# Optimization experiments

Measured on AMD Instinct MI355X. Metric: run time of the kernel, lower is better.

## Reference

```python
import jax, jax.numpy as jnp
from jax import lax
import numpy as np

B, T, F_IN, H = 64, 128, 12, 128  # batch, seq_len, input/output features, hidden


def _uinit(key, shape, fan):
    return jax.random.uniform(key, shape, jnp.float32, -1.0, 1.0) / np.float32(np.sqrt(fan))


def setup_inputs() -> dict:
    key = jax.random.key(0)
    ks = jax.random.split(key, 12)
    inp = {
        "x": jax.random.normal(ks[0], (B, T, F_IN), jnp.float32),
        # encoder LSTM (gate order i,f,g,o; b = b_ih + b_hh folded together)
        "enc_Wih": _uinit(ks[1], (4 * H, F_IN), H),
        "enc_Whh": _uinit(ks[2], (4 * H, H), H),
        "enc_b": _uinit(ks[3], (4 * H,), H),
        # decoder LSTM (input is the 12-dim teacher-forced x slice)
        "dec_Wih": _uinit(ks[4], (4 * H, F_IN), H),
        "dec_Whh": _uinit(ks[5], (4 * H, H), H),
        "dec_b": _uinit(ks[6], (4 * H,), H),
        # attention: Linear(2H -> H) with bias, then v: Linear(H -> 1, no bias)
        "attn_W": _uinit(ks[7], (H, 2 * H), 2 * H),
        "attn_b": _uinit(ks[8], (H,), 2 * H),
        "v_w": _uinit(ks[9], (H,), H),
        # output layer: Linear(2H -> F_IN)  (intended width; see notes)
        "out_W": _uinit(ks[10], (F_IN, 2 * H), 2 * H),
        "out_b": _uinit(ks[11], (F_IN,), 2 * H),
    }
    return inp


def _lstm_cell(xt, h, c, Wih, Whh, b):
    z = xt @ Wih.T + h @ Whh.T + b  # [B, 4H]
    i, f, g, o = jnp.split(z, 4, axis=-1)
    c = jax.nn.sigmoid(f) * c + jax.nn.sigmoid(i) * jnp.tanh(g)
    h = jax.nn.sigmoid(o) * jnp.tanh(c)
    return h, c


def reference(x, enc_Wih, enc_Whh, enc_b, dec_Wih, dec_Whh, dec_b,
              attn_W, attn_b, v_w, out_W, out_b):
    b_, t_, _ = x.shape
    hdim = enc_Whh.shape[1]
    xs = jnp.swapaxes(x, 0, 1)  # [T, B, F]
    h0 = jnp.zeros((b_, hdim), x.dtype)
    c0 = jnp.zeros((b_, hdim), x.dtype)

    def enc_step(carry, xt):
        h, c = carry
        h, c = _lstm_cell(xt, h, c, enc_Wih, enc_Whh, enc_b)
        return (h, c), h

    (hT, cT), enc_hs = lax.scan(enc_step, (h0, c0), xs)
    enc_out = jnp.swapaxes(enc_hs, 0, 1)  # [B, T, H]

    # split attn weight: cat(hidden, enc_out) @ W.T == hidden@W1.T + enc_out@W2.T
    W1, W2 = attn_W[:, :hdim], attn_W[:, hdim:]
    enc_proj = jnp.einsum("bth,gh->btg", enc_out, W2)  # precompute encoder side

    def dec_step(carry, xt):
        h, c = carry
        h, c = _lstm_cell(xt, h, c, dec_Wih, dec_Whh, dec_b)
        energy = jnp.tanh((h @ W1.T)[:, None, :] + enc_proj + attn_b)  # [B,T,H]
        score = jnp.einsum("bth,h->bt", energy, v_w)
        w = jax.nn.softmax(score, axis=1)  # attention over encoder time
        ctx = jnp.einsum("bt,bth->bh", w, enc_out)
        return (h, c), jnp.concatenate([h, ctx], axis=-1)  # [B, 2H]

    _, dec_ys = lax.scan(dec_step, (hT, cT), xs)
    dec_out = jnp.swapaxes(dec_ys, 0, 1)  # [B, T, 2H]
    return dec_out @ out_W.T + out_b  # [B, T, F]
```

## Files before the change

kernel.cpp:

```cpp
#include <hip/hip_runtime.h>
#include <hip/hip_bf16.h>

#define BB 64
#define TT 128
#define FIN 12
#define HH 128

#define LOG2E 1.4426950408889634f
#define TWO_LOG2E 2.8853900817779268f

__device__ __forceinline__ float fexp2(float x) { return __builtin_amdgcn_exp2f(x); }
__device__ __forceinline__ float frcp(float x)  { return __builtin_amdgcn_rcpf(x); }

__device__ __forceinline__ float tanh_f(float x) {
  return 1.0f - 2.0f * frcp(1.0f + fexp2(TWO_LOG2E * x));
}
__device__ __forceinline__ float sigm_f(float x) {
  return frcp(1.0f + fexp2(-LOG2E * x));
}

template <int CTRL>
__device__ __forceinline__ float dpp_addstage(float v) {
  int s = __builtin_amdgcn_update_dpp(0, __float_as_int(v), CTRL, 0xF, 0xF, true);
  return v + __int_as_float(s);
}
__device__ __forceinline__ float red8(float v) {
  v = dpp_addstage<0xB1>(v);
  v = dpp_addstage<0x4E>(v);
  v = dpp_addstage<0x141>(v);
  return v;
}

#define FMA4S(acc, s, v) do { \
  acc.x = fmaf((s), (v).x, acc.x); \
  acc.y = fmaf((s), (v).y, acc.y); \
  acc.z = fmaf((s), (v).z, acc.z); \
  acc.w = fmaf((s), (v).w, acc.w); } while (0)

#define ACC4(hv, wv, a) do { \
  a = fmaf((hv).x, (wv).x, a); a = fmaf((hv).y, (wv).y, a); \
  a = fmaf((hv).z, (wv).z, a); a = fmaf((hv).w, (wv).w, a); } while (0)

__device__ __forceinline__ void lstm_phase(
    const float* __restrict__ Wih, const float* __restrict__ Whh,
    const float* __restrict__ bias, float* __restrict__ Hout ,
    float* __restrict__ xs, float (*hbuf)[160], float* __restrict__ hist,
    const int tid, const int q, const int i, float& c)
{
  const int xo   = (q < 4) ? 3 * q : 0;
  const float xz = (q < 4) ? 1.0f : 0.0f;

  float4 wg[4][4];
  #pragma unroll
  for (int g = 0; g < 4; ++g)
    #pragma unroll
    for (int j = 0; j < 4; ++j)
      wg[g][j] = *(const float4*)(Whh + ((g * HH + i) * HH) + 16 * q + 4 * j);

  float wx[4][3];
  #pragma unroll
  for (int g = 0; g < 4; ++g)
    #pragma unroll
    for (int j = 0; j < 3; ++j)
      wx[g][j] = Wih[(g * HH + i) * FIN + xo + j] * xz;

  const float bi = bias[i], bf = bias[HH + i], bg = bias[2 * HH + i], bo = bias[3 * HH + i];

  int ts = 0;
  #pragma unroll 1
  for (int half = 0; half < 2; ++half) {
    #pragma unroll 1
    for (int tt = 0; tt < 64; ++tt, ++ts) {
      const int t = half * 64 + tt;
      __syncthreads();
      const float* hb = (const float*)hbuf[ts & 1] + q * 20;
      float4 h0 = *(const float4*)(hb + 0);
      float4 h1 = *(const float4*)(hb + 4);
      float4 h2 = *(const float4*)(hb + 8);
      float4 h3 = *(const float4*)(hb + 12);

      const float* xt = xs + t * FIN + xo;
      float x0 = xt[0], x1 = xt[1], x2 = xt[2];
      float ai = wx[0][0] * x0 + wx[0][1] * x1 + wx[0][2] * x2;
      float af = wx[1][0] * x0 + wx[1][1] * x1 + wx[1][2] * x2;
      float ag = wx[2][0] * x0 + wx[2][1] * x1 + wx[2][2] * x2;
      float ao = wx[3][0] * x0 + wx[3][1] * x1 + wx[3][2] * x2;

      ACC4(h0, wg[0][0], ai); ACC4(h0, wg[1][0], af); ACC4(h0, wg[2][0], ag); ACC4(h0, wg[3][0], ao);
      ACC4(h1, wg[0][1], ai); ACC4(h1, wg[1][1], af); ACC4(h1, wg[2][1], ag); ACC4(h1, wg[3][1], ao);
      ACC4(h2, wg[0][2], ai); ACC4(h2, wg[1][2], af); ACC4(h2, wg[2][2], ag); ACC4(h2, wg[3][2], ao);
      ACC4(h3, wg[0][3], ai); ACC4(h3, wg[1][3], af); ACC4(h3, wg[2][3], ag); ACC4(h3, wg[3][3], ao);

      ai = red8(ai); af = red8(af); ag = red8(ag); ao = red8(ao);

      if (q == 0) {
        float zi = sigm_f(ai + bi);
        float zf = sigm_f(af + bf);
        float zg = tanh_f(ag + bg);
        float zo = sigm_f(ao + bo);
        c = fmaf(zf, c, zi * zg);
        float hn = zo * tanh_f(c);
        hbuf[(ts + 1) & 1][(i >> 4) * 20 + (i & 15)] = hn;
        hist[tt * HH + i] = hn;
      }
    }
    __syncthreads();
    {
      float4* dst = (float4*)(Hout + (size_t)(half * 64) * HH);
      const float4* src = (const float4*)hist;
      dst[tid]        = src[tid];
      dst[tid + 1024] = src[tid + 1024];
    }
  }
}

__global__ __launch_bounds__(1024, 4) void lstm_enc_kernel(
    const float* __restrict__ x,
    const float* __restrict__ eWih, const float* __restrict__ eWhh, const float* __restrict__ eb,
    float* __restrict__ encH, float* __restrict__ cbuf)
{
  const int b   = blockIdx.x;
  const int tid = threadIdx.x;
  const int q   = tid & 7;
  const int i   = tid >> 3;

  __shared__ __align__(16) float xs[TT * FIN];
  __shared__ __align__(16) float hbuf[2][160];
  __shared__ __align__(16) float hist[64 * HH];

  if (tid < (TT * FIN / 4))
    ((float4*)xs)[tid] = ((const float4*)(x + (size_t)b * TT * FIN))[tid];
  if (tid < 320) ((float*)hbuf)[tid] = 0.0f;
  float c = 0.0f;

  lstm_phase(eWih, eWhh, eb, encH + (size_t)b * TT * HH, xs, hbuf, hist, tid, q, i, c);

  if (q == 0) cbuf[b * HH + i] = c;
}

__global__ __launch_bounds__(1024, 4) void lstm_dec_p_kernel(
    const float* __restrict__ x,
    const float* __restrict__ dWih, const float* __restrict__ dWhh, const float* __restrict__ db,
    const float* __restrict__ attnW,
    const float* __restrict__ encH, const float* __restrict__ cbuf,
    float* __restrict__ decH, float* __restrict__ Pbuf)
{
  __shared__ __align__(16) float smem[12416];
  const int tid = threadIdx.x;

  if (blockIdx.x < 64) {
    const int b = blockIdx.x;
    const int q = tid & 7;
    const int i = tid >> 3;
    float* xs           = smem;
    float (*hbuf)[160]  = (float(*)[160])(smem + 1536);
    float* hist         = smem + 1856;

    if (tid < (TT * FIN / 4))
      ((float4*)xs)[tid] = ((const float4*)(x + (size_t)b * TT * FIN))[tid];
    if (tid < 128) {
      float hv = encH[((size_t)b * TT + 127) * HH + tid];
      hbuf[0][(tid >> 4) * 20 + (tid & 15)] = hv;
    }
    float c = 0.0f;
    if (q == 0) c = cbuf[b * HH + i];

    lstm_phase(dWih, dWhh, db, decH + (size_t)b * TT * HH, xs, hbuf, hist, tid, q, i, c);
  } else {
    const int pb = blockIdx.x - 64;
    const int b  = pb & 63;
    const int r0 = (pb >> 6) * 64;
    float* WT = smem;
    float* Xt = smem + 4224;

    const float* X = encH + ((size_t)b * TT + r0) * HH;
    ((float4*)Xt)[tid]        = ((const float4*)X)[tid];
    ((float4*)Xt)[tid + 1024] = ((const float4*)X)[tid + 1024];

    const float* W = attnW + HH;
    const int hq = tid & 31, rr = tid >> 5;
    const int h0 = 4 * hq;

    float4 acc0 = make_float4(0.f, 0.f, 0.f, 0.f);
    float4 acc1 = acc0;

    #pragma unroll 1
    for (int kb = 0; kb < 4; ++kb) {
      __syncthreads();
      {
        int h = tid >> 3, koff = (tid & 7) * 4;
        float4 v = *(const float4*)(W + h * 256 + kb * 32 + koff);
        WT[(koff + 0) * 132 + h] = v.x;
        WT[(koff + 1) * 132 + h] = v.y;
        WT[(koff + 2) * 132 + h] = v.z;
        WT[(koff + 3) * 132 + h] = v.w;
      }
      __syncthreads();
      const float* xr0 = Xt + (2 * rr) * 128 + kb * 32;
      const float* xr1 = xr0 + 128;
      #pragma unroll
      for (int k4 = 0; k4 < 32; k4 += 4) {
        float4 xa = *(const float4*)(xr0 + k4);
        float4 xb = *(const float4*)(xr1 + k4);
        float4 w0 = *(const float4*)&WT[(k4 + 0) * 132 + h0];
        float4 w1 = *(const float4*)&WT[(k4 + 1) * 132 + h0];
        float4 w2 = *(const float4*)&WT[(k4 + 2) * 132 + h0];
        float4 w3 = *(const float4*)&WT[(k4 + 3) * 132 + h0];
        FMA4S(acc0, xa.x, w0); FMA4S(acc0, xa.y, w1);
        FMA4S(acc0, xa.z, w2); FMA4S(acc0, xa.w, w3);
        FMA4S(acc1, xb.x, w0); FMA4S(acc1, xb.y, w1);
        FMA4S(acc1, xb.z, w2); FMA4S(acc1, xb.w, w3);
      }
    }
    acc0.x = fexp2(TWO_LOG2E * acc0.x); acc0.y = fexp2(TWO_LOG2E * acc0.y);
    acc0.z = fexp2(TWO_LOG2E * acc0.z); acc0.w = fexp2(TWO_LOG2E * acc0.w);
    acc1.x = fexp2(TWO_LOG2E * acc1.x); acc1.y = fexp2(TWO_LOG2E * acc1.y);
    acc1.z = fexp2(TWO_LOG2E * acc1.z); acc1.w = fexp2(TWO_LOG2E * acc1.w);
    float* O = Pbuf + ((size_t)b * TT + r0) * HH;
    *(float4*)(O + (2 * rr) * 128 + h0)     = acc0;
    *(float4*)(O + (2 * rr + 1) * 128 + h0) = acc1;
  }
}

#define AST 132

__global__ __launch_bounds__(512, 2) void attn_kernel(
    const float* __restrict__ encH, const float* __restrict__ decH,
    const float* __restrict__ Pbuf,
    const float* __restrict__ attnW, const float* __restrict__ attnb,
    const float* __restrict__ vw, const float* __restrict__ outW,
    const float* __restrict__ outb, float* __restrict__ out)
{
  const int b  = blockIdx.x >> 3;
  const int s0 = (blockIdx.x & 7) * 16;
  const int tid = threadIdx.x;

  __shared__ __align__(16) float buf[64 * 128];
  __shared__ __align__(16) float a_lds[16 * AST];
  __shared__ __align__(16) float sc[16 * AST];
  __shared__ __align__(16) float dh[16 * 128];
  __shared__ __align__(16) float vl[HH];

  ((float4*)dh)[tid] = ((const float4*)(decH + ((size_t)b * TT + s0) * HH))[tid];
  if (tid < 32) ((float4*)vl)[tid] = ((const float4*)vw)[tid];

  const int u  = tid & 31;
  const int sl = tid >> 5;
  const int uq = u & 15;
  const int uh = u >> 4;

  __syncthreads();

  {
    const int h0 = 4 * u;
    float4 acc = *(const float4*)(attnb + h0);
    const float* drow = dh + sl * 128;
    const float* w0p = attnW + (size_t)(h0 + 0) * 256;
    const float* w1p = attnW + (size_t)(h0 + 1) * 256;
    const float* w2p = attnW + (size_t)(h0 + 2) * 256;
    const float* w3p = attnW + (size_t)(h0 + 3) * 256;
    #pragma unroll 8
    for (int k4 = 0; k4 < 128; k4 += 4) {
      float4 dv = *(const float4*)(drow + k4);
      float4 wa = *(const float4*)(w0p + k4);
      float4 wb = *(const float4*)(w1p + k4);
      float4 wc = *(const float4*)(w2p + k4);
      float4 wd = *(const float4*)(w3p + k4);
      ACC4(dv, wa, acc.x);
      ACC4(dv, wb, acc.y);
      ACC4(dv, wc, acc.z);
      ACC4(dv, wd, acc.w);
    }
    acc.x = fexp2(TWO_LOG2E * acc.x);
    acc.y = fexp2(TWO_LOG2E * acc.y);
    acc.z = fexp2(TWO_LOG2E * acc.z);
    acc.w = fexp2(TWO_LOG2E * acc.w);
    *(float4*)&a_lds[sl * AST + h0] = acc;
  }

  for (int half = 0; half < 2; ++half) {
    const int tbase = half * 64;
    __syncthreads();
    #pragma unroll
    for (int i = 0; i < 4; ++i) {
      int flat = i * 2048 + tid * 4;
      int tp = flat >> 7;
      int h0 = flat & 127;
      float4 v = *(const float4*)(Pbuf + ((size_t)b * TT + tbase + tp) * HH + h0);
      int tq = tp >> 2, tr = tp & 3;
      buf[(h0 + 0) * 64 + 4 * ((tq ^ ((h0 + 0) >> 2)) & 15) + tr] = v.x;
      buf[(h0 + 1) * 64 + 4 * ((tq ^ ((h0 + 1) >> 2)) & 15) + tr] = v.y;
      buf[(h0 + 2) * 64 + 4 * ((tq ^ ((h0 + 2) >> 2)) & 15) + tr] = v.z;
      buf[(h0 + 3) * 64 + 4 * ((tq ^ ((h0 + 3) >> 2)) & 15) + tr] = v.w;
    }
    __syncthreads();
    float4 acc = make_float4(0.f, 0.f, 0.f, 0.f);
    const float* earow = a_lds + sl * AST;
    #pragma unroll 4
    for (int hh = 0; hh < 64; hh += 4) {
      const int h = uh * 64 + hh;
      float4 ea = *(const float4*)&earow[h];
      float4 va = *(const float4*)&vl[h];
      const int xoff = 4 * ((uq ^ ((h >> 2) & 15)) & 15);
      float4 p0 = *(const float4*)&buf[(h + 0) * 64 + xoff];
      float4 p1 = *(const float4*)&buf[(h + 1) * 64 + xoff];
      float4 p2 = *(const float4*)&buf[(h + 2) * 64 + xoff];
      float4 p3 = *(const float4*)&buf[(h + 3) * 64 + xoff];
      acc.x = fmaf(va.x, frcp(fmaf(ea.x, p0.x, 1.f)), acc.x);
      acc.y = fmaf(va.x, frcp(fmaf(ea.x, p0.y, 1.f)), acc.y);
      acc.z = fmaf(va.x, frcp(fmaf(ea.x, p0.z, 1.f)), acc.z);
      acc.w = fmaf(va.x, frcp(fmaf(ea.x, p0.w, 1.f)), acc.w);
      acc.x = fmaf(va.y, frcp(fmaf(ea.y, p1.x, 1.f)), acc.x);
      acc.y = fmaf(va.y, frcp(fmaf(ea.y, p1.y, 1.f)), acc.y);
      acc.z = fmaf(va.y, frcp(fmaf(ea.y, p1.z, 1.f)), acc.z);
      acc.w = fmaf(va.y, frcp(fmaf(ea.y, p1.w, 1.f)), acc.w);
      acc.x = fmaf(va.z, frcp(fmaf(ea.z, p2.x, 1.f)), acc.x);
      acc.y = fmaf(va.z, frcp(fmaf(ea.z, p2.y, 1.f)), acc.y);
      acc.z = fmaf(va.z, frcp(fmaf(ea.z, p2.z, 1.f)), acc.z);
      acc.w = fmaf(va.z, frcp(fmaf(ea.z, p2.w, 1.f)), acc.w);
      acc.x = fmaf(va.w, frcp(fmaf(ea.w, p3.x, 1.f)), acc.x);
      acc.y = fmaf(va.w, frcp(fmaf(ea.w, p3.y, 1.f)), acc.y);
      acc.z = fmaf(va.w, frcp(fmaf(ea.w, p3.z, 1.f)), acc.z);
      acc.w = fmaf(va.w, frcp(fmaf(ea.w, p3.w, 1.f)), acc.w);
    }
    acc.x += __shfl_xor(acc.x, 16, 64);
    acc.y += __shfl_xor(acc.y, 16, 64);
    acc.z += __shfl_xor(acc.z, 16, 64);
    acc.w += __shfl_xor(acc.w, 16, 64);
    if (uh == 0) {
      float4 o;
      o.x = -2.f * acc.x; o.y = -2.f * acc.y;
      o.z = -2.f * acc.z; o.w = -2.f * acc.w;
      *(float4*)&sc[sl * AST + tbase + 4 * uq] = o;
    }
  }
  __syncthreads();

  {
    float4 sv = *(const float4*)&sc[sl * AST + 4 * u];
    float mx = fmaxf(fmaxf(sv.x, sv.y), fmaxf(sv.z, sv.w));
    #pragma unroll
    for (int msk = 1; msk <= 16; msk <<= 1) mx = fmaxf(mx, __shfl_xor(mx, msk, 64));
    float4 e;
    e.x = fexp2(LOG2E * (sv.x - mx));
    e.y = fexp2(LOG2E * (sv.y - mx));
    e.z = fexp2(LOG2E * (sv.z - mx));
    e.w = fexp2(LOG2E * (sv.w - mx));
    float sm = (e.x + e.y) + (e.z + e.w);
    #pragma unroll
    for (int msk = 1; msk <= 16; msk <<= 1) sm += __shfl_xor(sm, msk, 64);
    float r = frcp(sm);
    e.x *= r; e.y *= r; e.z *= r; e.w *= r;
    *(float4*)&sc[sl * AST + 4 * u] = e;
  }

  float4 ctx = make_float4(0.f, 0.f, 0.f, 0.f);
  const int h0c = 4 * u;
  for (int half = 0; half < 2; ++half) {
    const int tbase = half * 64;
    __syncthreads();
    #pragma unroll
    for (int i = 0; i < 4; ++i) {
      int flat = i * 2048 + tid * 4;
      int tp = flat >> 7;
      int hh0 = flat & 127;
      *(float4*)&buf[tp * 128 + hh0] =
          *(const float4*)(encH + ((size_t)b * TT + tbase + tp) * HH + hh0);
    }
    __syncthreads();
    const float* wrow = sc + sl * AST + tbase;
    #pragma unroll 8
    for (int tp = 0; tp < 64; ++tp) {
      float wt = wrow[tp];
      float4 e4 = *(const float4*)&buf[tp * 128 + h0c];
      FMA4S(ctx, wt, e4);
    }
  }
  __syncthreads();
  *(float4*)&a_lds[sl * AST + h0c] = ctx;
  __syncthreads();

  if (tid < 192) {
    int s = tid / 12, f = tid % 12;
    float acc = outb[f];
    const float4* w4 = (const float4*)(outW + f * 256);
    const float4* d4 = (const float4*)(dh + s * 128);
    const float4* c4 = (const float4*)(a_lds + s * AST);
    #pragma unroll
    for (int k = 0; k < 32; ++k) {
      float4 wv = w4[k], dv = d4[k];
      acc = fmaf(wv.x, dv.x, acc); acc = fmaf(wv.y, dv.y, acc);
      acc = fmaf(wv.z, dv.z, acc); acc = fmaf(wv.w, dv.w, acc);
    }
    #pragma unroll
    for (int k = 0; k < 32; ++k) {
      float4 wv = w4[32 + k], cv = c4[k];
      acc = fmaf(wv.x, cv.x, acc); acc = fmaf(wv.y, cv.y, acc);
      acc = fmaf(wv.z, cv.z, acc); acc = fmaf(wv.w, cv.w, acc);
    }
    out[((size_t)b * TT + s0 + s) * FIN + f] = acc;
  }
}

extern "C" void kernel_launch(void* const* d_in, const int* in_sizes, int n_in,
                              void* d_out, int out_size, void* d_ws, size_t ws_size,
                              hipStream_t stream)
{
  const float* x     = (const float*)d_in[0];
  const float* eWih  = (const float*)d_in[1];
  const float* eWhh  = (const float*)d_in[2];
  const float* eb    = (const float*)d_in[3];
  const float* dWih  = (const float*)d_in[4];
  const float* dWhh  = (const float*)d_in[5];
  const float* db    = (const float*)d_in[6];
  const float* attnW = (const float*)d_in[7];
  const float* attnb = (const float*)d_in[8];
  const float* vw    = (const float*)d_in[9];
  const float* outW  = (const float*)d_in[10];
  const float* outb  = (const float*)d_in[11];
  float* out = (float*)d_out;

  float* ws   = (float*)d_ws;
  const size_t SEG = (size_t)BB * TT * HH;
  float* encH = ws;
  float* decH = ws + SEG;
  float* Pbuf = ws + 2 * SEG;
  float* cbuf = ws + 3 * SEG;

  lstm_enc_kernel<<<64, 1024, 0, stream>>>(x, eWih, eWhh, eb, encH, cbuf);
  lstm_dec_p_kernel<<<192, 1024, 0, stream>>>(x, dWih, dWhh, db, attnW, encH, cbuf, decH, Pbuf);
  attn_kernel<<<512, 512, 0, stream>>>(encH, decH, Pbuf, attnW, attnb, vw, outW, outb, out);
}
```

Baseline: 364.8 us.

## Use packed FMA in LSTM recurrence and split decoder attention projection into own kernel

The recurrent matvec in the LSTM step now uses v_pk_fma_f32 on float pairs with separate accumulators, halving FMA instruction count and shortening dependency chains in the serial loop. The decoder-side attention projection (h@W1+b, then exp) moves out of attn_kernel into a new projA_kernel that stages W transposed in shared memory and writes an intermediate buffer, which attn_kernel then loads. The encoder's final cell state is passed through the first row of decH instead of a separate buffer. This adds a kernel launch and an extra global round trip for the projected values.

```diff
diff --git a/kernel.cpp b/kernel.cpp
--- a/kernel.cpp
+++ b/kernel.cpp
@@ -8,6 +8,9 @@
 
 #define LOG2E 1.4426950408889634f
 #define TWO_LOG2E 2.8853900817779268f
+
+typedef float f2v __attribute__((ext_vector_type(2)));
+union F4 { float4 v; f2v h[2]; };
 
 __device__ __forceinline__ float fexp2(float x) { return __builtin_amdgcn_exp2f(x); }
 __device__ __forceinline__ float frcp(float x)  { return __builtin_amdgcn_rcpf(x); }
@@ -31,6 +34,9 @@
   return v;
 }
 
+#define PKFMA(acc, hh, ww) \
+  asm("v_pk_fma_f32 %0, %1, %2, %0" : "+v"(acc) : "v"(hh), "v"(ww))
+
 #define FMA4S(acc, s, v) do { \
   acc.x = fmaf((s), (v).x, acc.x); \
   acc.y = fmaf((s), (v).y, acc.y); \
@@ -50,12 +56,12 @@
   const int xo   = (q < 4) ? 3 * q : 0;
   const float xz = (q < 4) ? 1.0f : 0.0f;
 
-  float4 wg[4][4];
+  F4 wg[4][4];
   #pragma unroll
   for (int g = 0; g < 4; ++g)
     #pragma unroll
     for (int j = 0; j < 4; ++j)
-      wg[g][j] = *(const float4*)(Whh + ((g * HH + i) * HH) + 16 * q + 4 * j);
+      wg[g][j].v = *(const float4*)(Whh + ((g * HH + i) * HH) + 16 * q + 4 * j);
 
   float wx[4][3];
   #pragma unroll
@@ -74,10 +80,11 @@
       const int t = half * 64 + tt;
       __syncthreads();
       const float* hb = (const float*)hbuf[ts & 1] + q * 20;
-      float4 h0 = *(const float4*)(hb + 0);
-      float4 h1 = *(const float4*)(hb + 4);
-      float4 h2 = *(const float4*)(hb + 8);
-      float4 h3 = *(const float4*)(hb + 12);
+      F4 H[4];
+      H[0].v = *(const float4*)(hb + 0);
+      H[1].v = *(const float4*)(hb + 4);
+      H[2].v = *(const float4*)(hb + 8);
+      H[3].v = *(const float4*)(hb + 12);
 
       const float* xt = xs + t * FIN + xo;
       float x0 = xt[0], x1 = xt[1], x2 = xt[2];
@@ -86,10 +93,16 @@
       float ag = wx[2][0] * x0 + wx[2][1] * x1 + wx[2][2] * x2;
       float ao = wx[3][0] * x0 + wx[3][1] * x1 + wx[3][2] * x2;
 
-      ACC4(h0, wg[0][0], ai); ACC4(h0, wg[1][0], af); ACC4(h0, wg[2][0], ag); ACC4(h0, wg[3][0], ao);
-      ACC4(h1, wg[0][1], ai); ACC4(h1, wg[1][1], af); ACC4(h1, wg[2][1], ag); ACC4(h1, wg[3][1], ao);
-      ACC4(h2, wg[0][2], ai); ACC4(h2, wg[1][2], af); ACC4(h2, wg[2][2], ag); ACC4(h2, wg[3][2], ao);
-      ACC4(h3, wg[0][3], ai); ACC4(h3, wg[1][3], af); ACC4(h3, wg[2][3], ag); ACC4(h3, wg[3][3], ao);
+      f2v A0 = {0.f, 0.f}, A1 = {0.f, 0.f}, A2 = {0.f, 0.f}, A3 = {0.f, 0.f};
+      #pragma unroll
+      for (int j = 0; j < 4; ++j) {
+        PKFMA(A0, H[j].h[0], wg[0][j].h[0]); PKFMA(A0, H[j].h[1], wg[0][j].h[1]);
+        PKFMA(A1, H[j].h[0], wg[1][j].h[0]); PKFMA(A1, H[j].h[1], wg[1][j].h[1]);
+        PKFMA(A2, H[j].h[0], wg[2][j].h[0]); PKFMA(A2, H[j].h[1], wg[2][j].h[1]);
+        PKFMA(A3, H[j].h[0], wg[3][j].h[0]); PKFMA(A3, H[j].h[1], wg[3][j].h[1]);
+      }
+      ai += A0.x + A0.y; af += A1.x + A1.y;
+      ag += A2.x + A2.y; ao += A3.x + A3.y;
 
       ai = red8(ai); af = red8(af); ag = red8(ag); ao = red8(ao);
 
@@ -117,7 +130,7 @@
 __global__ __launch_bounds__(1024, 4) void lstm_enc_kernel(
     const float* __restrict__ x,
     const float* __restrict__ eWih, const float* __restrict__ eWhh, const float* __restrict__ eb,
-    float* __restrict__ encH, float* __restrict__ cbuf)
+    float* __restrict__ encH, float* __restrict__ decH)
 {
   const int b   = blockIdx.x;
   const int tid = threadIdx.x;
@@ -135,14 +148,14 @@
 
   lstm_phase(eWih, eWhh, eb, encH + (size_t)b * TT * HH, xs, hbuf, hist, tid, q, i, c);
 
-  if (q == 0) cbuf[b * HH + i] = c;
+  if (q == 0) decH[(size_t)b * TT * HH + i] = c;
 }
 
 __global__ __launch_bounds__(1024, 4) void lstm_dec_p_kernel(
     const float* __restrict__ x,
     const float* __restrict__ dWih, const float* __restrict__ dWhh, const float* __restrict__ db,
     const float* __restrict__ attnW,
-    const float* __restrict__ encH, const float* __restrict__ cbuf,
+    const float* __restrict__ encH,
     float* __restrict__ decH, float* __restrict__ Pbuf)
 {
   __shared__ __align__(16) float smem[12416];
@@ -163,7 +176,7 @@
       hbuf[0][(tid >> 4) * 20 + (tid & 15)] = hv;
     }
     float c = 0.0f;
-    if (q == 0) c = cbuf[b * HH + i];
+    if (q == 0) c = decH[(size_t)b * TT * HH + i];
 
     lstm_phase(dWih, dWhh, db, decH + (size_t)b * TT * HH, xs, hbuf, hist, tid, q, i, c);
   } else {
@@ -222,12 +235,74 @@
   }
 }
 
+__global__ __launch_bounds__(256, 2) void projA_kernel(
+    const float* __restrict__ decH, const float* __restrict__ attnW,
+    const float* __restrict__ attnb, float* __restrict__ Abuf)
+{
+  const int b  = blockIdx.x & 63;
+  const int r0 = (blockIdx.x >> 6) * 16;
+  const int tid = threadIdx.x;
+
+  __shared__ __align__(16) float WT[64 * 128];
+  __shared__ __align__(16) float Xt[16 * 128];
+
+  const float* X = decH + ((size_t)b * TT + r0) * HH;
+  const float* W = attnW;
+
+  ((float4*)Xt)[tid]       = ((const float4*)X)[tid];
+  ((float4*)Xt)[256 + tid] = ((const float4*)X)[256 + tid];
+
+  const int hq = tid & 31, rr = tid >> 5;
+  const int h0 = 4 * hq;
+
+  float4 acc0 = *(const float4*)(attnb + h0);
+  float4 acc1 = acc0;
+
+  for (int kb = 0; kb < 2; ++kb) {
+    __syncthreads();
+    {
+      int h = tid >> 1, koff = (tid & 1) * 32;
+      #pragma unroll
+      for (int j = 0; j < 8; ++j) {
+        float4 v = *(const float4*)(W + h * 256 + kb * 64 + koff + 4 * j);
+        int kp = koff + 4 * j;
+        WT[(kp + 0) * 128 + h] = v.x;
+        WT[(kp + 1) * 128 + h] = v.y;
+        WT[(kp + 2) * 128 + h] = v.z;
+        WT[(kp + 3) * 128 + h] = v.w;
+      }
+    }
+    __syncthreads();
+    const float* xr0 = Xt + (2 * rr) * 128 + kb * 64;
+    const float* xr1 = xr0 + 128;
+    #pragma unroll
+    for (int k4 = 0; k4 < 64; k4 += 4) {
+      float4 xa = *(const float4*)(xr0 + k4);
+      float4 xb = *(const float4*)(xr1 + k4);
+      float4 w0 = *(const float4*)&WT[(k4 + 0) * 128 + h0];
+      float4 w1 = *(const float4*)&WT[(k4 + 1) * 128 + h0];
+      float4 w2 = *(const float4*)&WT[(k4 + 2) * 128 + h0];
+      float4 w3 = *(const float4*)&WT[(k4 + 3) * 128 + h0];
+      FMA4S(acc0, xa.x, w0); FMA4S(acc0, xa.y, w1);
+      FMA4S(acc0, xa.z, w2); FMA4S(acc0, xa.w, w3);
+      FMA4S(acc1, xb.x, w0); FMA4S(acc1, xb.y, w1);
+      FMA4S(acc1, xb.z, w2); FMA4S(acc1, xb.w, w3);
+    }
+  }
+  acc0.x = fexp2(TWO_LOG2E * acc0.x); acc0.y = fexp2(TWO_LOG2E * acc0.y);
+  acc0.z = fexp2(TWO_LOG2E * acc0.z); acc0.w = fexp2(TWO_LOG2E * acc0.w);
+  acc1.x = fexp2(TWO_LOG2E * acc1.x); acc1.y = fexp2(TWO_LOG2E * acc1.y);
+  acc1.z = fexp2(TWO_LOG2E * acc1.z); acc1.w = fexp2(TWO_LOG2E * acc1.w);
+  float* O = Abuf + ((size_t)b * TT + r0) * HH;
+  *(float4*)(O + (2 * rr) * 128 + h0)     = acc0;
+  *(float4*)(O + (2 * rr + 1) * 128 + h0) = acc1;
+}
+
 #define AST 132
 
 __global__ __launch_bounds__(512, 2) void attn_kernel(
     const float* __restrict__ encH, const float* __restrict__ decH,
-    const float* __restrict__ Pbuf,
-    const float* __restrict__ attnW, const float* __restrict__ attnb,
+    const float* __restrict__ Pbuf, const float* __restrict__ Abuf,
     const float* __restrict__ vw, const float* __restrict__ outW,
     const float* __restrict__ outb, float* __restrict__ out)
 {
@@ -243,40 +318,16 @@
 
   ((float4*)dh)[tid] = ((const float4*)(decH + ((size_t)b * TT + s0) * HH))[tid];
   if (tid < 32) ((float4*)vl)[tid] = ((const float4*)vw)[tid];
+  {
+    int r = tid >> 5, c4 = (tid & 31) * 4;
+    float4 av = *(const float4*)(Abuf + ((size_t)b * TT + s0 + r) * HH + c4);
+    *(float4*)&a_lds[r * AST + c4] = av;
+  }
 
   const int u  = tid & 31;
   const int sl = tid >> 5;
   const int uq = u & 15;
   const int uh = u >> 4;
-
-  __syncthreads();
-
-  {
-    const int h0 = 4 * u;
-    float4 acc = *(const float4*)(attnb + h0);
-    const float* drow = dh + sl * 128;
-    const float* w0p = attnW + (size_t)(h0 + 0) * 256;
-    const float* w1p = attnW + (size_t)(h0 + 1) * 256;
-    const float* w2p = attnW + (size_t)(h0 + 2) * 256;
-    const float* w3p = attnW + (size_t)(h0 + 3) * 256;
-    #pragma unroll 8
-    for (int k4 = 0; k4 < 128; k4 += 4) {
-      float4 dv = *(const float4*)(drow + k4);
-      float4 wa = *(const float4*)(w0p + k4);
-      float4 wb = *(const float4*)(w1p + k4);
-      float4 wc = *(const float4*)(w2p + k4);
-      float4 wd = *(const float4*)(w3p + k4);
-      ACC4(dv, wa, acc.x);
-      ACC4(dv, wb, acc.y);
-      ACC4(dv, wc, acc.z);
-      ACC4(dv, wd, acc.w);
-    }
-    acc.x = fexp2(TWO_LOG2E * acc.x);
-    acc.y = fexp2(TWO_LOG2E * acc.y);
-    acc.z = fexp2(TWO_LOG2E * acc.z);
-    acc.w = fexp2(TWO_LOG2E * acc.w);
-    *(float4*)&a_lds[sl * AST + h0] = acc;
-  }
 
   for (int half = 0; half < 2; ++half) {
     const int tbase = half * 64;
@@ -425,9 +476,10 @@
   float* encH = ws;
   float* decH = ws + SEG;
   float* Pbuf = ws + 2 * SEG;
-  float* cbuf = ws + 3 * SEG;
-
-  lstm_enc_kernel<<<64, 1024, 0, stream>>>(x, eWih, eWhh, eb, encH, cbuf);
-  lstm_dec_p_kernel<<<192, 1024, 0, stream>>>(x, dWih, dWhh, db, attnW, encH, cbuf, decH, Pbuf);
-  attn_kernel<<<512, 512, 0, stream>>>(encH, decH, Pbuf, attnW, attnb, vw, outW, outb, out);
-}
+  float* Abuf = ws + 3 * SEG;
+
+  lstm_enc_kernel<<<64, 1024, 0, stream>>>(x, eWih, eWhh, eb, encH, decH);
+  lstm_dec_p_kernel<<<192, 1024, 0, stream>>>(x, dWih, dWhh, db, attnW, encH, decH, Pbuf);
+  projA_kernel<<<512, 256, 0, stream>>>(decH, attnW, attnb, Abuf);
+  attn_kernel<<<512, 512, 0, stream>>>(encH, decH, Pbuf, Abuf, vw, outW, outb, out);
+}
```

Result: faster. 355.7 us (-2.5%).

## Fuse attention and output projection into the decoder recurrence with step pipelining

Applied to the files above, without the earlier changes.

Removes the separate attention kernel and runs attention scoring, softmax normalisation and the output projection inside the per-batch decoder loop. The work is staggered across timesteps so that the score, the context and the LSTM step of neighbouring steps share one barrier per iteration. The context-times-output-weight product is rewritten as a weighted sum of per-timestep encoder projections, which a new prep kernel precomputes. The softmax skips the max-subtraction and uses bounded exponentials instead. This removes the decH round trip and the large attention launch, but it adds per-step work to the serial recurrence, whose critical path gets longer.

```diff
diff --git a/kernel.cpp b/kernel.cpp
--- a/kernel.cpp
+++ b/kernel.cpp
@@ -41,12 +41,25 @@
   a = fmaf((hv).x, (wv).x, a); a = fmaf((hv).y, (wv).y, a); \
   a = fmaf((hv).z, (wv).z, a); a = fmaf((hv).w, (wv).w, a); } while (0)
 
-__device__ __forceinline__ void lstm_phase(
-    const float* __restrict__ Wih, const float* __restrict__ Whh,
-    const float* __restrict__ bias, float* __restrict__ Hout ,
-    float* __restrict__ xs, float (*hbuf)[160], float* __restrict__ hist,
-    const int tid, const int q, const int i, float& c)
+__global__ __launch_bounds__(1024, 4) void lstm_enc_kernel(
+    const float* __restrict__ x,
+    const float* __restrict__ eWih, const float* __restrict__ eWhh, const float* __restrict__ eb,
+    float* __restrict__ encH, float* __restrict__ cbuf)
 {
+  const int b   = blockIdx.x;
+  const int tid = threadIdx.x;
+  const int q   = tid & 7;
+  const int i   = tid >> 3;
+
+  __shared__ __align__(16) float xs[TT * FIN];
+  __shared__ __align__(16) float hbuf[2][160];
+  __shared__ __align__(16) float hist[64 * HH];
+
+  if (tid < (TT * FIN / 4))
+    ((float4*)xs)[tid] = ((const float4*)(x + (size_t)b * TT * FIN))[tid];
+  if (tid < 320) ((float*)hbuf)[tid] = 0.0f;
+  float c = 0.0f;
+
   const int xo   = (q < 4) ? 3 * q : 0;
   const float xz = (q < 4) ? 1.0f : 0.0f;
 
@@ -55,17 +68,16 @@
   for (int g = 0; g < 4; ++g)
     #pragma unroll
     for (int j = 0; j < 4; ++j)
-      wg[g][j] = *(const float4*)(Whh + ((g * HH + i) * HH) + 16 * q + 4 * j);
-
+      wg[g][j] = *(const float4*)(eWhh + ((g * HH + i) * HH) + 16 * q + 4 * j);
   float wx[4][3];
   #pragma unroll
   for (int g = 0; g < 4; ++g)
     #pragma unroll
     for (int j = 0; j < 3; ++j)
-      wx[g][j] = Wih[(g * HH + i) * FIN + xo + j] * xz;
-
-  const float bi = bias[i], bf = bias[HH + i], bg = bias[2 * HH + i], bo = bias[3 * HH + i];
-
+      wx[g][j] = eWih[(g * HH + i) * FIN + xo + j] * xz;
+  const float bi = eb[i], bf = eb[HH + i], bg = eb[2 * HH + i], bo = eb[3 * HH + i];
+
+  float* Hout = encH + (size_t)b * TT * HH;
   int ts = 0;
   #pragma unroll 1
   for (int half = 0; half < 2; ++half) {
@@ -112,62 +124,19 @@
       dst[tid + 1024] = src[tid + 1024];
     }
   }
-}
-
-__global__ __launch_bounds__(1024, 4) void lstm_enc_kernel(
-    const float* __restrict__ x,
-    const float* __restrict__ eWih, const float* __restrict__ eWhh, const float* __restrict__ eb,
-    float* __restrict__ encH, float* __restrict__ cbuf)
-{
-  const int b   = blockIdx.x;
-  const int tid = threadIdx.x;
-  const int q   = tid & 7;
-  const int i   = tid >> 3;
-
-  __shared__ __align__(16) float xs[TT * FIN];
-  __shared__ __align__(16) float hbuf[2][160];
-  __shared__ __align__(16) float hist[64 * HH];
-
-  if (tid < (TT * FIN / 4))
-    ((float4*)xs)[tid] = ((const float4*)(x + (size_t)b * TT * FIN))[tid];
-  if (tid < 320) ((float*)hbuf)[tid] = 0.0f;
-  float c = 0.0f;
-
-  lstm_phase(eWih, eWhh, eb, encH + (size_t)b * TT * HH, xs, hbuf, hist, tid, q, i, c);
-
   if (q == 0) cbuf[b * HH + i] = c;
 }
 
-__global__ __launch_bounds__(1024, 4) void lstm_dec_p_kernel(
-    const float* __restrict__ x,
-    const float* __restrict__ dWih, const float* __restrict__ dWhh, const float* __restrict__ db,
-    const float* __restrict__ attnW,
-    const float* __restrict__ encH, const float* __restrict__ cbuf,
-    float* __restrict__ decH, float* __restrict__ Pbuf)
+__global__ __launch_bounds__(1024, 4) void prep_kernel(
+    const float* __restrict__ attnW, const float* __restrict__ outW,
+    const float* __restrict__ encH,
+    float* __restrict__ Pbuf, float* __restrict__ y2buf)
 {
   __shared__ __align__(16) float smem[12416];
   const int tid = threadIdx.x;
 
-  if (blockIdx.x < 64) {
-    const int b = blockIdx.x;
-    const int q = tid & 7;
-    const int i = tid >> 3;
-    float* xs           = smem;
-    float (*hbuf)[160]  = (float(*)[160])(smem + 1536);
-    float* hist         = smem + 1856;
-
-    if (tid < (TT * FIN / 4))
-      ((float4*)xs)[tid] = ((const float4*)(x + (size_t)b * TT * FIN))[tid];
-    if (tid < 128) {
-      float hv = encH[((size_t)b * TT + 127) * HH + tid];
-      hbuf[0][(tid >> 4) * 20 + (tid & 15)] = hv;
-    }
-    float c = 0.0f;
-    if (q == 0) c = cbuf[b * HH + i];
-
-    lstm_phase(dWih, dWhh, db, decH + (size_t)b * TT * HH, xs, hbuf, hist, tid, q, i, c);
-  } else {
-    const int pb = blockIdx.x - 64;
+  if (blockIdx.x < 128) {
+    const int pb = blockIdx.x;
     const int b  = pb & 63;
     const int r0 = (pb >> 6) * 64;
     float* WT = smem;
@@ -219,187 +188,217 @@
     float* O = Pbuf + ((size_t)b * TT + r0) * HH;
     *(float4*)(O + (2 * rr) * 128 + h0)     = acc0;
     *(float4*)(O + (2 * rr + 1) * 128 + h0) = acc1;
-  }
-}
-
-#define AST 132
-
-__global__ __launch_bounds__(512, 2) void attn_kernel(
-    const float* __restrict__ encH, const float* __restrict__ decH,
-    const float* __restrict__ Pbuf,
+  } else {
+    const int b = blockIdx.x - 128;
+    float* w2l = smem;
+    if (tid < 384) {
+      int f = tid >> 5, k = (tid & 31) * 4;
+      float4 wv = *(const float4*)(outW + f * 256 + 128 + k);
+      *(float4*)&w2l[f * 132 + k] = wv;
+    }
+    __syncthreads();
+    for (int j = tid; j < TT * 12; j += 1024) {
+      int t = j / 12, f = j - 12 * t;
+      const float* er = encH + ((size_t)b * TT + t) * HH;
+      const float* wr = w2l + f * 132;
+      float a = 0.f;
+      #pragma unroll 8
+      for (int k = 0; k < 32; ++k) {
+        float4 ev = *(const float4*)(er + 4 * k);
+        float4 wv = *(const float4*)(wr + 4 * k);
+        ACC4(ev, wv, a);
+      }
+      y2buf[b * (TT * 16) + t * 16 + f] = a;
+    }
+  }
+}
+
+#define EPST 132
+
+__global__ __launch_bounds__(1024, 4) void dec_attn_kernel(
+    const float* __restrict__ x,
+    const float* __restrict__ dWih, const float* __restrict__ dWhh, const float* __restrict__ db,
     const float* __restrict__ attnW, const float* __restrict__ attnb,
     const float* __restrict__ vw, const float* __restrict__ outW,
-    const float* __restrict__ outb, float* __restrict__ out)
+    const float* __restrict__ outb,
+    const float* __restrict__ encH, const float* __restrict__ cbuf,
+    const float* __restrict__ Pbuf, const float* __restrict__ y2buf,
+    float* __restrict__ out)
 {
-  const int b  = blockIdx.x >> 3;
-  const int s0 = (blockIdx.x & 7) * 16;
+  const int b   = blockIdx.x;
   const int tid = threadIdx.x;
-
-  __shared__ __align__(16) float buf[64 * 128];
-  __shared__ __align__(16) float a_lds[16 * AST];
-  __shared__ __align__(16) float sc[16 * AST];
-  __shared__ __align__(16) float dh[16 * 128];
+  const int q   = tid & 7;
+  const int i   = tid >> 3;
+
+  __shared__ __align__(16) float xs[TT * FIN];
+  __shared__ __align__(16) float hbuf[2][160];
+  __shared__ __align__(16) float ep[128 * EPST];
+  __shared__ __align__(16) float y2t[12 * EPST];
   __shared__ __align__(16) float vl[HH];
-
-  ((float4*)dh)[tid] = ((const float4*)(decH + ((size_t)b * TT + s0) * HH))[tid];
+  __shared__ __align__(16) float ea[2][HH];
+  __shared__ __align__(16) float erow[2][HH];
+  __shared__ __align__(16) float obuf[TT * FIN];
+
+  if (tid < (TT * FIN / 4))
+    ((float4*)xs)[tid] = ((const float4*)(x + (size_t)b * TT * FIN))[tid];
   if (tid < 32) ((float4*)vl)[tid] = ((const float4*)vw)[tid];
-
-  const int u  = tid & 31;
-  const int sl = tid >> 5;
-  const int uq = u & 15;
-  const int uh = u >> 4;
+  {
+    const float4* src = (const float4*)(Pbuf + (size_t)b * TT * HH);
+    #pragma unroll
+    for (int j = 0; j < 4; ++j) {
+      int idx = tid + j * 1024;
+      float4 v = src[idx];
+      int t = idx >> 5, c4 = (idx & 31) * 4;
+      *(float4*)&ep[t * EPST + c4] = v;
+    }
+  }
+  {
+    const float* src = y2buf + (size_t)b * (TT * 16);
+    for (int j = tid; j < TT * 12; j += 1024) {
+      int f = j >> 7, t = j & 127;
+      y2t[f * EPST + t] = src[t * 16 + f];
+    }
+  }
+  if (tid < 128) {
+    float hv = encH[((size_t)b * TT + 127) * HH + tid];
+    hbuf[0][(tid >> 4) * 20 + (tid & 15)] = hv;
+  }
+  float c = 0.0f;
+  if (q == 0) c = cbuf[b * HH + i];
+
+  const int xo   = (q < 4) ? 3 * q : 0;
+  const float xz = (q < 4) ? 1.0f : 0.0f;
+  float4 wg[4][4];
+  #pragma unroll
+  for (int g = 0; g < 4; ++g)
+    #pragma unroll
+    for (int j = 0; j < 4; ++j)
+      wg[g][j] = *(const float4*)(dWhh + ((g * HH + i) * HH) + 16 * q + 4 * j);
+  float wx[4][3];
+  #pragma unroll
+  for (int g = 0; g < 4; ++g)
+    #pragma unroll
+    for (int j = 0; j < 3; ++j)
+      wx[g][j] = dWih[(g * HH + i) * FIN + xo + j] * xz;
+  const float bi = db[i], bf = db[HH + i], bg = db[2 * HH + i], bo = db[3 * HH + i];
+  const float abias = attnb[i];
+  float ob = 0.f;
+  if (i < FIN) ob = outb[i];
+  float o1a = 0.f, o1b = 0.f;
+
+  #pragma unroll 1
+  for (int ts = 0; ts < 131; ++ts) {
+    __syncthreads();
+
+    if (ts >= 3) {
+      if (i < FIN) {
+        const float* er = erow[(ts & 1) ^ 1];
+        float o2p = 0.f, zp = 0.f;
+        const float* yr = y2t + i * EPST + 16 * q;
+        #pragma unroll
+        for (int j = 0; j < 4; ++j) {
+          float4 ev = *(const float4*)(er + 16 * q + 4 * j);
+          float4 yv = *(const float4*)(yr + 4 * j);
+          zp += (ev.x + ev.y) + (ev.z + ev.w);
+          ACC4(ev, yv, o2p);
+        }
+        o2p = red8(o2p); zp = red8(zp);
+        if (q == 0)
+          obuf[(ts - 3) * FIN + i] = ob + o1b + o2p * frcp(zp);
+      }
+    }
+
+    if (ts >= 2 && ts <= 129) {
+      const float* eap = ea[(ts & 1) ^ 1] + 16 * q;
+      const float* epp = ep + i * EPST + 16 * q;
+      const float* vp  = vl + 16 * q;
+      float sE = 0.f;
+      #pragma unroll
+      for (int j = 0; j < 4; ++j) {
+        float4 eav = *(const float4*)(eap + 4 * j);
+        float4 epv = *(const float4*)(epp + 4 * j);
+        float4 vv  = *(const float4*)(vp + 4 * j);
+        sE = fmaf(vv.x, frcp(fmaf(eav.x, epv.x, 1.f)), sE);
+        sE = fmaf(vv.y, frcp(fmaf(eav.y, epv.y, 1.f)), sE);
+        sE = fmaf(vv.z, frcp(fmaf(eav.z, epv.z, 1.f)), sE);
+        sE = fmaf(vv.w, frcp(fmaf(eav.w, epv.w, 1.f)), sE);
+      }
+      sE = red8(sE);
+      if (q == 0)
+        erow[ts & 1][i] = fexp2(LOG2E * (-2.f * sE));
+    }
+
+    if (ts <= 128) {
+      const float* hb = (const float*)hbuf[ts & 1] + q * 20;
+      float4 h0 = *(const float4*)(hb + 0);
+      float4 h1 = *(const float4*)(hb + 4);
+      float4 h2 = *(const float4*)(hb + 8);
+      float4 h3 = *(const float4*)(hb + 12);
+
+      if (ts < 128) {
+        const float* xt = xs + ts * FIN + xo;
+        float x0 = xt[0], x1 = xt[1], x2 = xt[2];
+        float ai = wx[0][0] * x0 + wx[0][1] * x1 + wx[0][2] * x2;
+        float af = wx[1][0] * x0 + wx[1][1] * x1 + wx[1][2] * x2;
+        float ag = wx[2][0] * x0 + wx[2][1] * x1 + wx[2][2] * x2;
+        float ao = wx[3][0] * x0 + wx[3][1] * x1 + wx[3][2] * x2;
+
+        ACC4(h0, wg[0][0], ai); ACC4(h0, wg[1][0], af); ACC4(h0, wg[2][0], ag); ACC4(h0, wg[3][0], ao);
+        ACC4(h1, wg[0][1], ai); ACC4(h1, wg[1][1], af); ACC4(h1, wg[2][1], ag); ACC4(h1, wg[3][1], ao);
+        ACC4(h2, wg[0][2], ai); ACC4(h2, wg[1][2], af); ACC4(h2, wg[2][2], ag); ACC4(h2, wg[3][2], ao);
+        ACC4(h3, wg[0][3], ai); ACC4(h3, wg[1][3], af); ACC4(h3, wg[2][3], ag); ACC4(h3, wg[3][3], ao);
+
+        ai = red8(ai); af = red8(af); ag = red8(ag); ao = red8(ao);
+
+        if (q == 0) {
+          float zi = sigm_f(ai + bi);
+          float zf = sigm_f(af + bf);
+          float zg = tanh_f(ag + bg);
+          float zo = sigm_f(ao + bo);
+          c = fmaf(zf, c, zi * zg);
+          float hn = zo * tanh_f(c);
+          hbuf[(ts + 1) & 1][(i >> 4) * 20 + (i & 15)] = hn;
+        }
+      }
+
+      if (ts >= 1) {
+        const float* wA = attnW + i * 256 + 16 * q;
+        float aA = 0.f;
+        {
+          float4 w0 = *(const float4*)(wA + 0);
+          float4 w1 = *(const float4*)(wA + 4);
+          float4 w2 = *(const float4*)(wA + 8);
+          float4 w3 = *(const float4*)(wA + 12);
+          ACC4(h0, w0, aA); ACC4(h1, w1, aA);
+          ACC4(h2, w2, aA); ACC4(h3, w3, aA);
+        }
+        aA = red8(aA);
+
+        float aO = 0.f;
+        if (i < FIN) {
+          const float* wO = outW + i * 256 + 16 * q;
+          float4 w0 = *(const float4*)(wO + 0);
+          float4 w1 = *(const float4*)(wO + 4);
+          float4 w2 = *(const float4*)(wO + 8);
+          float4 w3 = *(const float4*)(wO + 12);
+          ACC4(h0, w0, aO); ACC4(h1, w1, aO);
+          ACC4(h2, w2, aO); ACC4(h3, w3, aO);
+          aO = red8(aO);
+        }
+
+        if (q == 0) {
+          ea[ts & 1][i] = fexp2(TWO_LOG2E * (aA + abias));
+          if (i < FIN) { o1b = o1a; o1a = aO; }
+        }
+      }
+    } else if (ts == 129) {
+      if (q == 0 && i < FIN) o1b = o1a;
+    }
+  }
 
   __syncthreads();
-
-  {
-    const int h0 = 4 * u;
-    float4 acc = *(const float4*)(attnb + h0);
-    const float* drow = dh + sl * 128;
-    const float* w0p = attnW + (size_t)(h0 + 0) * 256;
-    const float* w1p = attnW + (size_t)(h0 + 1) * 256;
-    const float* w2p = attnW + (size_t)(h0 + 2) * 256;
-    const float* w3p = attnW + (size_t)(h0 + 3) * 256;
-    #pragma unroll 8
-    for (int k4 = 0; k4 < 128; k4 += 4) {
-      float4 dv = *(const float4*)(drow + k4);
-      float4 wa = *(const float4*)(w0p + k4);
-      float4 wb = *(const float4*)(w1p + k4);
-      float4 wc = *(const float4*)(w2p + k4);
-      float4 wd = *(const float4*)(w3p + k4);
-      ACC4(dv, wa, acc.x);
-      ACC4(dv, wb, acc.y);
-      ACC4(dv, wc, acc.z);
-      ACC4(dv, wd, acc.w);
-    }
-    acc.x = fexp2(TWO_LOG2E * acc.x);
-    acc.y = fexp2(TWO_LOG2E * acc.y);
-    acc.z = fexp2(TWO_LOG2E * acc.z);
-    acc.w = fexp2(TWO_LOG2E * acc.w);
-    *(float4*)&a_lds[sl * AST + h0] = acc;
-  }
-
-  for (int half = 0; half < 2; ++half) {
-    const int tbase = half * 64;
-    __syncthreads();
-    #pragma unroll
-    for (int i = 0; i < 4; ++i) {
-      int flat = i * 2048 + tid * 4;
-      int tp = flat >> 7;
-      int h0 = flat & 127;
-      float4 v = *(const float4*)(Pbuf + ((size_t)b * TT + tbase + tp) * HH + h0);
-      int tq = tp >> 2, tr = tp & 3;
-      buf[(h0 + 0) * 64 + 4 * ((tq ^ ((h0 + 0) >> 2)) & 15) + tr] = v.x;
-      buf[(h0 + 1) * 64 + 4 * ((tq ^ ((h0 + 1) >> 2)) & 15) + tr] = v.y;
-      buf[(h0 + 2) * 64 + 4 * ((tq ^ ((h0 + 2) >> 2)) & 15) + tr] = v.z;
-      buf[(h0 + 3) * 64 + 4 * ((tq ^ ((h0 + 3) >> 2)) & 15) + tr] = v.w;
-    }
-    __syncthreads();
-    float4 acc = make_float4(0.f, 0.f, 0.f, 0.f);
-    const float* earow = a_lds + sl * AST;
-    #pragma unroll 4
-    for (int hh = 0; hh < 64; hh += 4) {
-      const int h = uh * 64 + hh;
-      float4 ea = *(const float4*)&earow[h];
-      float4 va = *(const float4*)&vl[h];
-      const int xoff = 4 * ((uq ^ ((h >> 2) & 15)) & 15);
-      float4 p0 = *(const float4*)&buf[(h + 0) * 64 + xoff];
-      float4 p1 = *(const float4*)&buf[(h + 1) * 64 + xoff];
-      float4 p2 = *(const float4*)&buf[(h + 2) * 64 + xoff];
-      float4 p3 = *(const float4*)&buf[(h + 3) * 64 + xoff];
-      acc.x = fmaf(va.x, frcp(fmaf(ea.x, p0.x, 1.f)), acc.x);
-      acc.y = fmaf(va.x, frcp(fmaf(ea.x, p0.y, 1.f)), acc.y);
-      acc.z = fmaf(va.x, frcp(fmaf(ea.x, p0.z, 1.f)), acc.z);
-      acc.w = fmaf(va.x, frcp(fmaf(ea.x, p0.w, 1.f)), acc.w);
-      acc.x = fmaf(va.y, frcp(fmaf(ea.y, p1.x, 1.f)), acc.x);
-      acc.y = fmaf(va.y, frcp(fmaf(ea.y, p1.y, 1.f)), acc.y);
-      acc.z = fmaf(va.y, frcp(fmaf(ea.y, p1.z, 1.f)), acc.z);
-      acc.w = fmaf(va.y, frcp(fmaf(ea.y, p1.w, 1.f)), acc.w);
-      acc.x = fmaf(va.z, frcp(fmaf(ea.z, p2.x, 1.f)), acc.x);
-      acc.y = fmaf(va.z, frcp(fmaf(ea.z, p2.y, 1.f)), acc.y);
-      acc.z = fmaf(va.z, frcp(fmaf(ea.z, p2.z, 1.f)), acc.z);
-      acc.w = fmaf(va.z, frcp(fmaf(ea.z, p2.w, 1.f)), acc.w);
-      acc.x = fmaf(va.w, frcp(fmaf(ea.w, p3.x, 1.f)), acc.x);
-      acc.y = fmaf(va.w, frcp(fmaf(ea.w, p3.y, 1.f)), acc.y);
-      acc.z = fmaf(va.w, frcp(fmaf(ea.w, p3.z, 1.f)), acc.z);
-      acc.w = fmaf(va.w, frcp(fmaf(ea.w, p3.w, 1.f)), acc.w);
-    }
-    acc.x += __shfl_xor(acc.x, 16, 64);
-    acc.y += __shfl_xor(acc.y, 16, 64);
-    acc.z += __shfl_xor(acc.z, 16, 64);
-    acc.w += __shfl_xor(acc.w, 16, 64);
-    if (uh == 0) {
-      float4 o;
-      o.x = -2.f * acc.x; o.y = -2.f * acc.y;
-      o.z = -2.f * acc.z; o.w = -2.f * acc.w;
-      *(float4*)&sc[sl * AST + tbase + 4 * uq] = o;
-    }
-  }
-  __syncthreads();
-
-  {
-    float4 sv = *(const float4*)&sc[sl * AST + 4 * u];
-    float mx = fmaxf(fmaxf(sv.x, sv.y), fmaxf(sv.z, sv.w));
-    #pragma unroll
-    for (int msk = 1; msk <= 16; msk <<= 1) mx = fmaxf(mx, __shfl_xor(mx, msk, 64));
-    float4 e;
-    e.x = fexp2(LOG2E * (sv.x - mx));
-    e.y = fexp2(LOG2E * (sv.y - mx));
-    e.z = fexp2(LOG2E * (sv.z - mx));
-    e.w = fexp2(LOG2E * (sv.w - mx));
-    float sm = (e.x + e.y) + (e.z + e.w);
-    #pragma unroll
-    for (int msk = 1; msk <= 16; msk <<= 1) sm += __shfl_xor(sm, msk, 64);
-    float r = frcp(sm);
-    e.x *= r; e.y *= r; e.z *= r; e.w *= r;
-    *(float4*)&sc[sl * AST + 4 * u] = e;
-  }
-
-  float4 ctx = make_float4(0.f, 0.f, 0.f, 0.f);
-  const int h0c = 4 * u;
-  for (int half = 0; half < 2; ++half) {
-    const int tbase = half * 64;
-    __syncthreads();
-    #pragma unroll
-    for (int i = 0; i < 4; ++i) {
-      int flat = i * 2048 + tid * 4;
-      int tp = flat >> 7;
-      int hh0 = flat & 127;
-      *(float4*)&buf[tp * 128 + hh0] =
-          *(const float4*)(encH + ((size_t)b * TT + tbase + tp) * HH + hh0);
-    }
-    __syncthreads();
-    const float* wrow = sc + sl * AST + tbase;
-    #pragma unroll 8
-    for (int tp = 0; tp < 64; ++tp) {
-      float wt = wrow[tp];
-      float4 e4 = *(const float4*)&buf[tp * 128 + h0c];
-      FMA4S(ctx, wt, e4);
-    }
-  }
-  __syncthreads();
-  *(float4*)&a_lds[sl * AST + h0c] = ctx;
-  __syncthreads();
-
-  if (tid < 192) {
-    int s = tid / 12, f = tid % 12;
-    float acc = outb[f];
-    const float4* w4 = (const float4*)(outW + f * 256);
-    const float4* d4 = (const float4*)(dh + s * 128);
-    const float4* c4 = (const float4*)(a_lds + s * AST);
-    #pragma unroll
-    for (int k = 0; k < 32; ++k) {
-      float4 wv = w4[k], dv = d4[k];
-      acc = fmaf(wv.x, dv.x, acc); acc = fmaf(wv.y, dv.y, acc);
-      acc = fmaf(wv.z, dv.z, acc); acc = fmaf(wv.w, dv.w, acc);
-    }
-    #pragma unroll
-    for (int k = 0; k < 32; ++k) {
-      float4 wv = w4[32 + k], cv = c4[k];
-      acc = fmaf(wv.x, cv.x, acc); acc = fmaf(wv.y, cv.y, acc);
-      acc = fmaf(wv.z, cv.z, acc); acc = fmaf(wv.w, cv.w, acc);
-    }
-    out[((size_t)b * TT + s0 + s) * FIN + f] = acc;
-  }
+  if (tid < 384)
+    ((float4*)(out + (size_t)b * TT * FIN))[tid] = ((const float4*)obuf)[tid];
 }
 
 extern "C" void kernel_launch(void* const* d_in, const int* in_sizes, int n_in,
@@ -422,12 +421,13 @@
 
   float* ws   = (float*)d_ws;
   const size_t SEG = (size_t)BB * TT * HH;
-  float* encH = ws;
-  float* decH = ws + SEG;
-  float* Pbuf = ws + 2 * SEG;
-  float* cbuf = ws + 3 * SEG;
+  float* encH  = ws;
+  float* Pbuf  = ws + SEG;
+  float* y2buf = ws + 2 * SEG;
+  float* cbuf  = ws + 2 * SEG + (size_t)BB * TT * 16;
 
   lstm_enc_kernel<<<64, 1024, 0, stream>>>(x, eWih, eWhh, eb, encH, cbuf);
-  lstm_dec_p_kernel<<<192, 1024, 0, stream>>>(x, dWih, dWhh, db, attnW, encH, cbuf, decH, Pbuf);
-  attn_kernel<<<512, 512, 0, stream>>>(encH, decH, Pbuf, attnW, attnb, vw, outW, outb, out);
-}
+  prep_kernel<<<192, 1024, 0, stream>>>(attnW, outW, encH, Pbuf, y2buf);
+  dec_attn_kernel<<<64, 1024, 0, stream>>>(x, dWih, dWhh, db, attnW, attnb, vw,
+                                           outW, outb, encH, cbuf, Pbuf, y2buf, out);
+}
```

Result: slower. 660.9 us (+81.2%).
